# Optimization experiments

Measured on AMD Instinct MI355X. Metric: run time of the kernel, lower is better.

The kernel has to match this reference:

```python
import jax, jax.numpy as jnp
import numpy as np

N_NODES = 100000
N_EDGES = 3200000
IN_CH = 512
HID_CH = 40   # 2 * out_channels
OUT_CH = 20


def setup_inputs() -> dict:
    key = jax.random.key(0)
    k1, k2, k3, k4, k5, k6 = jax.random.split(key, 6)
    x = jax.random.normal(k1, (N_NODES, IN_CH), dtype=jnp.float32)
    edge_index = jax.random.randint(k2, (2, N_EDGES), 0, N_NODES, dtype=jnp.int32)
    # Glorot-style init for GCN weights, zero bias (PyG default)
    W1 = jax.random.normal(k3, (IN_CH, HID_CH), dtype=jnp.float32) * (1.0 / np.sqrt(IN_CH))
    b1 = jnp.zeros((HID_CH,), dtype=jnp.float32)
    W2 = jax.random.normal(k4, (HID_CH, OUT_CH), dtype=jnp.float32) * (1.0 / np.sqrt(HID_CH))
    b2 = jnp.zeros((OUT_CH,), dtype=jnp.float32)
    return {"x": x, "edge_index": edge_index, "W1": W1, "b1": b1, "W2": W2, "b2": b2}


def _gcn_conv(x, src, dst, W, b):
    """PyG GCNConv: add self-loops, symmetric norm, linear, scatter-add, bias."""
    n = x.shape[0]
    loops = jnp.arange(n, dtype=src.dtype)
    src = jnp.concatenate([src, loops])
    dst = jnp.concatenate([dst, loops])
    # in-degree over A + I (self-loops guarantee deg >= 1)
    deg = jax.ops.segment_sum(jnp.ones(src.shape[0], x.dtype), dst, num_segments=n)
    dinv = jax.lax.rsqrt(deg)
    norm = dinv[src] * dinv[dst]               # [E+N]
    h = x @ W                                   # [N, out] GEMM before aggregation
    msg = h[src] * norm[:, None]                # gather + scale
    out = jax.ops.segment_sum(msg, dst, num_segments=n)  # scatter-add at targets
    return out + b


def reference(x, edge_index, W1, b1, W2, b2):
    src, dst = edge_index[0], edge_index[1]
    h = jax.nn.relu(_gcn_conv(x, src, dst, W1, b1))
    # dropout is identity in eval mode (training=False)
    return _gcn_conv(h, src, dst, W2, b2)
```

## Files before the change

### kernel.cpp

```cpp
#include <hip/hip_runtime.h>
#include <cstddef>

static constexpr int NN   = 100000;
static constexpr int NE   = 3200000;
static constexpr int CIN  = 512;
static constexpr int CHID = 40;
static constexpr int COUT = 20;

static constexpr int NCH    = 32;
static constexpr int CHUNK_E = NE / NCH;
static constexpr int NRANGE = 8;
static constexpr int RANGE  = NN / NRANGE;

typedef float f32x4 __attribute__((ext_vector_type(4)));


__global__ __launch_bounds__(1024) void k_histA(const int* __restrict__ dst,
                                                int* __restrict__ cntb) {
  __shared__ int hc[RANGE];
  const int c  = blockIdx.x >> 3;
  const int r0 = (blockIdx.x & 7) * RANGE;
  for (int i = threadIdx.x; i < RANGE; i += 1024) hc[i] = 0;
  __syncthreads();
  const int base = c * (CHUNK_E / 4);
  const int end  = base + CHUNK_E / 4;
  for (int i = base + (int)threadIdx.x; i < end; i += 1024) {
    const int4 d = ((const int4*)dst)[i];
    if ((unsigned)(d.x - r0) < (unsigned)RANGE) atomicAdd(&hc[d.x - r0], 1);
    if ((unsigned)(d.y - r0) < (unsigned)RANGE) atomicAdd(&hc[d.y - r0], 1);
    if ((unsigned)(d.z - r0) < (unsigned)RANGE) atomicAdd(&hc[d.z - r0], 1);
    if ((unsigned)(d.w - r0) < (unsigned)RANGE) atomicAdd(&hc[d.w - r0], 1);
  }
  __syncthreads();
  int* __restrict__ outp = cntb + (size_t)c * NN + r0;
  for (int i = threadIdx.x; i < RANGE; i += 1024) outp[i] = hc[i];
}

__global__ __launch_bounds__(256) void k_merge(int* __restrict__ cntb, int* __restrict__ cnt, int n) {
  const int i = blockIdx.x * 256 + threadIdx.x;
  if (i >= n) return;
  int s = 0;
#pragma unroll 8
  for (int b = 0; b < NCH; ++b) {
    int* p = cntb + (size_t)b * NN + i;
    const int t = *p;
    *p = s;
    s += t;
  }
  cnt[i] = s;
}

__global__ __launch_bounds__(256) void k_scanA(const int* __restrict__ cnt, int* __restrict__ excl,
                                               int* __restrict__ bsums, float* __restrict__ dinv, int n) {
  __shared__ int sdata[256];
  const int t = threadIdx.x;
  const int base = blockIdx.x * 1024 + t * 4;
  int v[4];
#pragma unroll
  for (int j = 0; j < 4; ++j) {
    const int i = base + j;
    v[j] = (i < n) ? cnt[i] : 0;
    if (i < n) dinv[i] = rsqrtf((float)(v[j] + 1));
  }
  const int s4 = v[0] + v[1] + v[2] + v[3];
  sdata[t] = s4;
  __syncthreads();
  for (int off = 1; off < 256; off <<= 1) {
    int val = 0;
    if (t >= off) val = sdata[t - off];
    __syncthreads();
    sdata[t] += val;
    __syncthreads();
  }
  int run = sdata[t] - s4;
#pragma unroll
  for (int j = 0; j < 4; ++j) {
    const int i = base + j;
    if (i < n) excl[i] = run;
    run += v[j];
  }
  if (t == 255) bsums[blockIdx.x] = sdata[255];
}

__global__ __launch_bounds__(256) void k_scanB(int* __restrict__ bsums, int nb) {
  __shared__ int sdata[256];
  const int t = threadIdx.x;
  const int v = (t < nb) ? bsums[t] : 0;
  sdata[t] = v;
  __syncthreads();
  for (int off = 1; off < 256; off <<= 1) {
    int val = 0;
    if (t >= off) val = sdata[t - off];
    __syncthreads();
    sdata[t] += val;
    __syncthreads();
  }
  if (t < nb) bsums[t] = sdata[t] - v;
}

__global__ __launch_bounds__(256) void k_scanC(int* __restrict__ rowptr, const int* __restrict__ boff,
                                               int n, int n_edges) {
  const int i = blockIdx.x * 256 + threadIdx.x;
  if (i < n) rowptr[i] += boff[i >> 10];
  if (i == 0) rowptr[n] = n_edges;
}

__global__ __launch_bounds__(1024) void k_histFill(const int* __restrict__ src,
                                                   const int* __restrict__ dst,
                                                   const int* __restrict__ rowptr,
                                                   const int* __restrict__ cntb,
                                                   int* __restrict__ csr_src) {
  __shared__ int hc[RANGE];
  const int c  = blockIdx.x >> 3;
  const int r0 = (blockIdx.x & 7) * RANGE;
  for (int i = threadIdx.x; i < RANGE; i += 1024) hc[i] = 0;
  __syncthreads();
  const int* __restrict__ cbo = cntb + (size_t)c * NN;
  const int base = c * (CHUNK_E / 4);
  const int end  = base + CHUNK_E / 4;
  for (int i = base + (int)threadIdx.x; i < end; i += 1024) {
    const int4 d = ((const int4*)dst)[i];
    const int4 s = ((const int4*)src)[i];
    if ((unsigned)(d.x - r0) < (unsigned)RANGE) {
      const int rk = atomicAdd(&hc[d.x - r0], 1);
      csr_src[rowptr[d.x] + cbo[d.x] + rk] = s.x;
    }
    if ((unsigned)(d.y - r0) < (unsigned)RANGE) {
      const int rk = atomicAdd(&hc[d.y - r0], 1);
      csr_src[rowptr[d.y] + cbo[d.y] + rk] = s.y;
    }
    if ((unsigned)(d.z - r0) < (unsigned)RANGE) {
      const int rk = atomicAdd(&hc[d.z - r0], 1);
      csr_src[rowptr[d.z] + cbo[d.z] + rk] = s.z;
    }
    if ((unsigned)(d.w - r0) < (unsigned)RANGE) {
      const int rk = atomicAdd(&hc[d.w - r0], 1);
      csr_src[rowptr[d.w] + cbo[d.w] + rk] = s.w;
    }
  }
}

__global__ __launch_bounds__(256) void k_gemm1(const float* __restrict__ x, const float* __restrict__ W,
                                               float* __restrict__ h, int n) {
  __shared__ float xt[64 * 128];
  const int t  = threadIdx.x;
  const int nd = t & 63;
  const int g  = __builtin_amdgcn_readfirstlane(t >> 6);
  const int block0 = blockIdx.x * 64;

  const int sn = t >> 5;
  const int c4 = t & 31;

  float acc[10];
#pragma unroll
  for (int j = 0; j < 10; ++j) acc[j] = 0.f;

  for (int kt = 0; kt < 4; ++kt) {
    f32x4 v[8];
#pragma unroll
    for (int r = 0; r < 8; ++r) {
      const int row = r * 8 + sn;
      int gn = block0 + row;
      if (gn >= n) gn = n - 1;
      v[r] = __builtin_nontemporal_load(
          ((const f32x4*)(x + (size_t)gn * CIN + kt * 128)) + c4);
    }
    if (kt) __syncthreads();
#pragma unroll
    for (int r = 0; r < 8; ++r) {
      const int row = r * 8 + sn;
      const int byte = row * 512 + ((c4 * 16) ^ ((row & 31) << 4));
      *(f32x4*)((char*)xt + byte) = v[r];
    }
    __syncthreads();

    const float* __restrict__ Wg = W + (size_t)kt * 128 * CHID + g * 10;
#pragma unroll 4
    for (int k4 = 0; k4 < 32; ++k4) {
      const int byte = nd * 512 + ((k4 * 16) ^ ((nd & 31) << 4));
      const f32x4 xv = *(const f32x4*)((const char*)xt + byte);
      const float* __restrict__ Wk = Wg + k4 * 4 * CHID;
#pragma unroll
      for (int j = 0; j < 10; ++j) acc[j] = fmaf(xv.x, Wk[j], acc[j]);
#pragma unroll
      for (int j = 0; j < 10; ++j) acc[j] = fmaf(xv.y, Wk[CHID + j], acc[j]);
#pragma unroll
      for (int j = 0; j < 10; ++j) acc[j] = fmaf(xv.z, Wk[2 * CHID + j], acc[j]);
#pragma unroll
      for (int j = 0; j < 10; ++j) acc[j] = fmaf(xv.w, Wk[3 * CHID + j], acc[j]);
    }
  }

  __syncthreads();
#pragma unroll
  for (int j = 0; j < 10; ++j) xt[nd * 44 + g * 10 + j] = acc[j];
  __syncthreads();
  for (int i = t; i < 640; i += 256) {
    const int row = i / 10;
    const int c   = i % 10;
    const int node = block0 + row;
    if (node < n)
      ((float4*)(h + (size_t)node * CHID))[c] = *(const float4*)&xt[row * 44 + c * 4];
  }
}

__global__ __launch_bounds__(256) void k_gemm2(const float* __restrict__ t1, const float* __restrict__ W,
                                               float* __restrict__ g, int n) {
  const int node = blockIdx.x * 256 + threadIdx.x;
  if (node >= n) return;
  const float4* __restrict__ r4 = (const float4*)(t1 + (size_t)node * CHID);
  float acc[COUT];
#pragma unroll
  for (int c = 0; c < COUT; ++c) acc[c] = 0.f;
#pragma unroll
  for (int kk = 0; kk < CHID / 4; ++kk) {
    const float4 xv = r4[kk];
    const float* __restrict__ Wk = W + kk * 4 * COUT;
#pragma unroll
    for (int c = 0; c < COUT; ++c) {
      float a = acc[c];
      a = fmaf(xv.x, Wk[c], a);
      a = fmaf(xv.y, Wk[COUT + c], a);
      a = fmaf(xv.z, Wk[2 * COUT + c], a);
      a = fmaf(xv.w, Wk[3 * COUT + c], a);
      acc[c] = a;
    }
  }
  float* __restrict__ o = g + (size_t)node * COUT;
#pragma unroll
  for (int c = 0; c < COUT; ++c) o[c] = acc[c];
}

__global__ __launch_bounds__(256) void k_agg40(const float* __restrict__ h, const int* __restrict__ rowptr,
                                               const int* __restrict__ csr_src, const float* __restrict__ dinv,
                                               const float* __restrict__ bias, float* __restrict__ out, int n) {
  const int wave = (blockIdx.x * 256 + (int)threadIdx.x) >> 6;
  const int lane = threadIdx.x & 63;
  const int sub  = lane / 20;
  const int cp   = lane % 20;
  const int node = wave * 3 + sub;
  if (sub >= 3 || node >= n) return;
  const float2* __restrict__ h2 = (const float2*)h;
  const int r0 = rowptr[node];
  const int r1 = rowptr[node + 1];
  const float dv = dinv[node];
  const float self_w = dv * dv;
  float2 acc = h2[(size_t)node * 20 + cp];
  acc.x *= self_w;
  acc.y *= self_w;
  int i = r0;
  for (; i + 4 <= r1; i += 4) {
    const int s0 = csr_src[i + 0];
    const int s1 = csr_src[i + 1];
    const int s2 = csr_src[i + 2];
    const int s3 = csr_src[i + 3];
    const float w0 = dinv[s0] * dv;
    const float w1 = dinv[s1] * dv;
    const float w2 = dinv[s2] * dv;
    const float w3 = dinv[s3] * dv;
    const float2 g0 = h2[(size_t)s0 * 20 + cp];
    const float2 g1 = h2[(size_t)s1 * 20 + cp];
    const float2 g2 = h2[(size_t)s2 * 20 + cp];
    const float2 g3 = h2[(size_t)s3 * 20 + cp];
    acc.x = fmaf(g0.x, w0, acc.x); acc.y = fmaf(g0.y, w0, acc.y);
    acc.x = fmaf(g1.x, w1, acc.x); acc.y = fmaf(g1.y, w1, acc.y);
    acc.x = fmaf(g2.x, w2, acc.x); acc.y = fmaf(g2.y, w2, acc.y);
    acc.x = fmaf(g3.x, w3, acc.x); acc.y = fmaf(g3.y, w3, acc.y);
  }
  for (; i < r1; ++i) {
    const int s = csr_src[i];
    const float w = dinv[s] * dv;
    const float2 g = h2[(size_t)s * 20 + cp];
    acc.x = fmaf(g.x, w, acc.x);
    acc.y = fmaf(g.y, w, acc.y);
  }
  const float2 bv = ((const float2*)bias)[cp];
  float2 v;
  v.x = fmaxf(acc.x + bv.x, 0.f);
  v.y = fmaxf(acc.y + bv.y, 0.f);
  ((float2*)out)[(size_t)node * 20 + cp] = v;
}

__global__ __launch_bounds__(256) void k_agg20(const float* __restrict__ h, const int* __restrict__ rowptr,
                                               const int* __restrict__ csr_src, const float* __restrict__ dinv,
                                               const float* __restrict__ bias, float* __restrict__ out, int n) {
  const int wave = (blockIdx.x * 256 + (int)threadIdx.x) >> 6;
  const int lane = threadIdx.x & 63;
  const int sub  = lane / 10;
  const int cp   = lane % 10;
  const int node = wave * 6 + sub;
  if (sub >= 6 || node >= n) return;
  const float2* __restrict__ h2 = (const float2*)h;
  const int r0 = rowptr[node];
  const int r1 = rowptr[node + 1];
  const float dv = dinv[node];
  const float self_w = dv * dv;
  float2 acc = h2[(size_t)node * 10 + cp];
  acc.x *= self_w;
  acc.y *= self_w;
  int i = r0;
  for (; i + 4 <= r1; i += 4) {
    const int s0 = csr_src[i + 0];
    const int s1 = csr_src[i + 1];
    const int s2 = csr_src[i + 2];
    const int s3 = csr_src[i + 3];
    const float w0 = dinv[s0] * dv;
    const float w1 = dinv[s1] * dv;
    const float w2 = dinv[s2] * dv;
    const float w3 = dinv[s3] * dv;
    const float2 g0 = h2[(size_t)s0 * 10 + cp];
    const float2 g1 = h2[(size_t)s1 * 10 + cp];
    const float2 g2 = h2[(size_t)s2 * 10 + cp];
    const float2 g3 = h2[(size_t)s3 * 10 + cp];
    acc.x = fmaf(g0.x, w0, acc.x); acc.y = fmaf(g0.y, w0, acc.y);
    acc.x = fmaf(g1.x, w1, acc.x); acc.y = fmaf(g1.y, w1, acc.y);
    acc.x = fmaf(g2.x, w2, acc.x); acc.y = fmaf(g2.y, w2, acc.y);
    acc.x = fmaf(g3.x, w3, acc.x); acc.y = fmaf(g3.y, w3, acc.y);
  }
  for (; i < r1; ++i) {
    const int s = csr_src[i];
    const float w = dinv[s] * dv;
    const float2 g = h2[(size_t)s * 10 + cp];
    acc.x = fmaf(g.x, w, acc.x);
    acc.y = fmaf(g.y, w, acc.y);
  }
  const float2 bv = ((const float2*)bias)[cp];
  float2 v;
  v.x = acc.x + bv.x;
  v.y = acc.y + bv.y;
  ((float2*)out)[(size_t)node * 10 + cp] = v;
}


extern "C" void kernel_launch(void* const* d_in, const int* in_sizes, int n_in,
                              void* d_out, int out_size, void* d_ws, size_t ws_size,
                              hipStream_t stream) {
  const float* x   = (const float*)d_in[0];
  const int*   ei  = (const int*)d_in[1];
  const float* W1  = (const float*)d_in[2];
  const float* b1  = (const float*)d_in[3];
  const float* W2  = (const float*)d_in[4];
  const float* b2  = (const float*)d_in[5];
  float* out = (float*)d_out;

  const int* srcp = ei;
  const int* dstp = ei + NE;

  char* ws = (char*)d_ws;
  size_t off = 0;
  auto take = [&](size_t bytes) -> char* {
    char* p = ws + off;
    off = (off + bytes + 255) & ~(size_t)255;
    return p;
  };
  int*   cnt     = (int*)take((size_t)NN * 4);
  int*   rowptr  = (int*)take((size_t)(NN + 1) * 4);
  float* dinv    = (float*)take((size_t)NN * 4);
  int*   bsums   = (int*)take(256 * 4);
  int*   cntb    = (int*)take((size_t)NCH * NN * 4);
  int*   csr_src = (int*)take((size_t)NE * 4);
  float* h1      = (float*)take((size_t)NN * CHID * 4);
  float* t1      = (float*)take((size_t)NN * CHID * 4);
  float* g2      = h1;

  (void)in_sizes; (void)n_in; (void)out_size; (void)ws_size;

  const int nb = (NN + 1023) / 1024;

  k_histA<<<NCH * NRANGE, 1024, 0, stream>>>(dstp, cntb);
  k_merge<<<(NN + 255) / 256, 256, 0, stream>>>(cntb, cnt, NN);
  k_scanA<<<nb, 256, 0, stream>>>(cnt, rowptr, bsums, dinv, NN);
  k_scanB<<<1, 256, 0, stream>>>(bsums, nb);
  k_scanC<<<(NN + 255) / 256, 256, 0, stream>>>(rowptr, bsums, NN, NE);
  k_histFill<<<NCH * NRANGE, 1024, 0, stream>>>(srcp, dstp, rowptr, cntb, csr_src);

  k_gemm1<<<(NN + 63) / 64, 256, 0, stream>>>(x, W1, h1, NN);
  const int nwaves1 = (NN + 2) / 3;
  k_agg40<<<(nwaves1 + 3) / 4, 256, 0, stream>>>(h1, rowptr, csr_src, dinv, b1, t1, NN);
  k_gemm2<<<(NN + 255) / 256, 256, 0, stream>>>(t1, W2, g2, NN);
  const int nwaves2 = (NN + 5) / 6;
  k_agg20<<<(nwaves2 + 3) / 4, 256, 0, stream>>>(g2, rowptr, csr_src, dinv, b2, out, NN);
}
```

Baseline: 689.0 us.

## Double-buffer LDS tiles in GEMM1 with register prefetch of next K slice

The first-layer GEMM now splits K into eight 64-wide slices instead of four 128-wide ones and keeps two LDS buffers. The global loads for the next slice are issued into registers before computing on the current one, then stored to the other buffer. This overlaps HBM reads of x with the FMA loop and cuts the barriers to one per slice. The cost is more loop iterations and slightly more register pressure from holding the prefetched vectors.

```diff
diff --git a/kernel.cpp b/kernel.cpp
--- a/kernel.cpp
+++ b/kernel.cpp
@@ -142,43 +142,53 @@
 
 __global__ __launch_bounds__(256) void k_gemm1(const float* __restrict__ x, const float* __restrict__ W,
                                                float* __restrict__ h, int n) {
-  __shared__ float xt[64 * 128];
+  __shared__ float xt[2][64 * 64];
   const int t  = threadIdx.x;
   const int nd = t & 63;
   const int g  = __builtin_amdgcn_readfirstlane(t >> 6);
   const int block0 = blockIdx.x * 64;
 
-  const int sn = t >> 5;
-  const int c4 = t & 31;
+  const int srow = t >> 4;
+  const int c4   = t & 15;
 
   float acc[10];
 #pragma unroll
   for (int j = 0; j < 10; ++j) acc[j] = 0.f;
 
-  for (int kt = 0; kt < 4; ++kt) {
-    f32x4 v[8];
-#pragma unroll
-    for (int r = 0; r < 8; ++r) {
-      const int row = r * 8 + sn;
-      int gn = block0 + row;
-      if (gn >= n) gn = n - 1;
-      v[r] = __builtin_nontemporal_load(
-          ((const f32x4*)(x + (size_t)gn * CIN + kt * 128)) + c4);
-    }
-    if (kt) __syncthreads();
-#pragma unroll
-    for (int r = 0; r < 8; ++r) {
-      const int row = r * 8 + sn;
-      const int byte = row * 512 + ((c4 * 16) ^ ((row & 31) << 4));
-      *(f32x4*)((char*)xt + byte) = v[r];
-    }
-    __syncthreads();
-
-    const float* __restrict__ Wg = W + (size_t)kt * 128 * CHID + g * 10;
+  f32x4 v[4];
+#pragma unroll
+  for (int r = 0; r < 4; ++r) {
+    const int row = r * 16 + srow;
+    int gn = block0 + row;
+    if (gn >= n) gn = n - 1;
+    v[r] = __builtin_nontemporal_load(((const f32x4*)(x + (size_t)gn * CIN)) + c4);
+  }
+#pragma unroll
+  for (int r = 0; r < 4; ++r) {
+    const int row = r * 16 + srow;
+    const int byte = row * 256 + ((c4 * 16) ^ ((row & 15) << 4));
+    *(f32x4*)((char*)&xt[0][0] + byte) = v[r];
+  }
+  __syncthreads();
+
+  for (int kt = 0; kt < 8; ++kt) {
+    if (kt < 7) {
+#pragma unroll
+      for (int r = 0; r < 4; ++r) {
+        const int row = r * 16 + srow;
+        int gn = block0 + row;
+        if (gn >= n) gn = n - 1;
+        v[r] = __builtin_nontemporal_load(
+            ((const f32x4*)(x + (size_t)gn * CIN + (kt + 1) * 64)) + c4);
+      }
+    }
+
+    const float* __restrict__ bufc = &xt[kt & 1][0];
+    const float* __restrict__ Wg = W + (size_t)kt * 64 * CHID + g * 10;
 #pragma unroll 4
-    for (int k4 = 0; k4 < 32; ++k4) {
-      const int byte = nd * 512 + ((k4 * 16) ^ ((nd & 31) << 4));
-      const f32x4 xv = *(const f32x4*)((const char*)xt + byte);
+    for (int k4 = 0; k4 < 16; ++k4) {
+      const int byte = nd * 256 + ((k4 * 16) ^ ((nd & 15) << 4));
+      const f32x4 xv = *(const f32x4*)((const char*)bufc + byte);
       const float* __restrict__ Wk = Wg + k4 * 4 * CHID;
 #pragma unroll
       for (int j = 0; j < 10; ++j) acc[j] = fmaf(xv.x, Wk[j], acc[j]);
@@ -189,18 +199,27 @@
 #pragma unroll
       for (int j = 0; j < 10; ++j) acc[j] = fmaf(xv.w, Wk[3 * CHID + j], acc[j]);
     }
-  }
-
-  __syncthreads();
-#pragma unroll
-  for (int j = 0; j < 10; ++j) xt[nd * 44 + g * 10 + j] = acc[j];
+
+    if (kt < 7) {
+#pragma unroll
+      for (int r = 0; r < 4; ++r) {
+        const int row = r * 16 + srow;
+        const int byte = row * 256 + ((c4 * 16) ^ ((row & 15) << 4));
+        *(f32x4*)((char*)&xt[(kt + 1) & 1][0] + byte) = v[r];
+      }
+      __syncthreads();
+    }
+  }
+
+#pragma unroll
+  for (int j = 0; j < 10; ++j) xt[0][nd * 44 + g * 10 + j] = acc[j];
   __syncthreads();
   for (int i = t; i < 640; i += 256) {
     const int row = i / 10;
     const int c   = i % 10;
     const int node = block0 + row;
     if (node < n)
-      ((float4*)(h + (size_t)node * CHID))[c] = *(const float4*)&xt[row * 44 + c * 4];
+      ((float4*)(h + (size_t)node * CHID))[c] = *(const float4*)&xt[0][row * 44 + c * 4];
   }
 }
 
```

After: 699.1 us. Within noise of the previous version (+1.5%).
